# Kernel tuning notes

Measured on AMD Instinct MI355X. Metric: run time of the kernel, lower is better.

The kernel has to match this reference:

```python
import jax, jax.numpy as jnp
import numpy as np
from jax import lax

IN_CH, OC, NUM_LAYER = 6, 16, 256
ENC_DIM = OC * 4  # 64
DECODE_LEN = 23
FLAT = 5184


def _conv3d(x, w, b):
    # x: (B,C,D,H,W), w: (O,I,3,3,3), padding 1, stride 1
    y = lax.conv_general_dilated(x, w, window_strides=(1, 1, 1),
                                 padding=((1, 1), (1, 1), (1, 1)),
                                 dimension_numbers=('NCDHW', 'OIDHW', 'NCDHW'))
    return y + b[None, :, None, None, None]


def _maxpool(x):
    # MaxPool3d kernel (2,2,1) stride (2,2,1) over (D,H,W)
    return lax.reduce_window(x, -jnp.inf, lax.max,
                             (1, 1, 2, 2, 1), (1, 1, 2, 2, 1), 'VALID')


def setup_inputs() -> dict:
    key = jax.random.key(0)
    ks = jax.random.split(key, 24)
    n = lambda k, s: jax.random.normal(k, s, dtype=jnp.float32) * 0.05
    z = lambda s: jnp.zeros(s, dtype=jnp.float32)
    return {
        'x': jax.random.normal(ks[0], (512, IN_CH, 24, 72, 3), dtype=jnp.float32),
        'w1': n(ks[1], (OC, IN_CH, 3, 3, 3)), 'b1': z((OC,)),
        'w2': n(ks[2], (OC * 2, OC, 3, 3, 3)), 'b2': z((OC * 2,)),
        'w3': n(ks[3], (OC * 4, OC * 2, 3, 3, 3)), 'b3': z((OC * 4,)),
        'wih1': n(ks[4], (NUM_LAYER, ENC_DIM)), 'whh1': n(ks[5], (NUM_LAYER, NUM_LAYER)),
        'bih1': z((NUM_LAYER,)), 'bhh1': z((NUM_LAYER,)),
        'wih2': n(ks[6], (NUM_LAYER, NUM_LAYER)), 'whh2': n(ks[7], (NUM_LAYER, NUM_LAYER)),
        'bih2': z((NUM_LAYER,)), 'bhh2': z((NUM_LAYER,)),
        'w_init_h': n(ks[8], (NUM_LAYER, ENC_DIM)), 'b_init_h': z((NUM_LAYER,)),
        'w_init_h2': n(ks[9], (NUM_LAYER, NUM_LAYER)), 'b_init_h2': z((NUM_LAYER,)),
        'w_fc': n(ks[10], (1, NUM_LAYER)), 'b_fc': z((1,)),
        'w_lin1': n(ks[11], (NUM_LAYER, FLAT)), 'b_lin1': z((NUM_LAYER,)),
        'w_lin2': n(ks[12], (12, NUM_LAYER)), 'b_lin2': z((12,)),
    }


def reference(x, w1, b1, w2, b2, w3, b3,
              wih1, whh1, bih1, bhh1, wih2, whh2, bih2, bhh2,
              w_init_h, b_init_h, w_init_h2, b_init_h2,
              w_fc, b_fc, w_lin1, b_lin1, w_lin2, b_lin2):
    # Encoder: three conv+relu+pool stages (dropout is identity at p=0.0)
    out = _maxpool(jax.nn.relu(_conv3d(x, w1, b1)))
    out = _maxpool(jax.nn.relu(_conv3d(out, w2, b2)))
    out = _maxpool(jax.nn.relu(_conv3d(out, w3, b3)))  # (B, 64, 3, 9, 3)
    out = out.transpose(0, 2, 3, 4, 1)  # (B, D, H, W, C)
    B, C = out.shape[0], out.shape[-1]
    enc = out.reshape(B, -1, C)
    mean_enc = enc.mean(axis=1)  # (B, enc_dim)

    h = mean_enc @ w_init_h.T + b_init_h
    h2 = h @ w_init_h2.T + b_init_h2

    # Precompute the input-to-hidden projection once (constant across steps)
    ih_const = mean_enc @ wih1.T + bih1 + bhh1

    def step(carry, _):
        h, h2 = carry
        h_new = jnp.tanh(ih_const + h @ whh1.T)
        h2_new = jnp.tanh(h_new @ wih2.T + bih2 + h2 @ whh2.T + bhh2)
        pred = h2_new @ w_fc.T + b_fc  # (B, 1)
        return (h_new, h2_new), pred

    _, preds = lax.scan(step, (h, h2), None, length=DECODE_LEN)  # (T, B, 1)
    predictions = preds.transpose(1, 0, 2)  # (B, 23, 1)

    flat = out.reshape(B, -1)  # (B, 5184) in permuted (D,H,W,C) order, same as torch
    out_c = jnp.tanh(flat @ w_lin1.T + b_lin1) @ w_lin2.T + b_lin2  # (B, 12)
    return predictions, out_c
```

## Files before the change

### kernel.cpp

```cpp
#include <hip/hip_runtime.h>
#include <hip/hip_bf16.h>

typedef __attribute__((ext_vector_type(8))) short short8;
typedef __attribute__((ext_vector_type(4))) short short4_t;
typedef __attribute__((ext_vector_type(4))) float floatx4;

#define OFF_B1P   0
#define OFF_B2P   1792
#define OFF_B3P   8960
#define OFF_WIHT  36608
#define OFF_WIH1T 52992
#define OFF_WI2B  69376
#define OFF_WHH1B 134912
#define OFF_WIH2B 167680
#define OFF_WHH2B 200448
#define OFF_WL1P  233216
#define OFF_ME    896768
#define OFF_H0BF  929536
#define OFF_H2    1060608
#define OFF_IHC   1191680
#define OFF_P1    1322752
#define OFF_T1    1322752
#define OFF_Y     2377728
#define OFF_HSEQ  5392384
#define OFF_P2    6631168
#define OFF_P3BF  9285376

#define S2_H 88
#define S2_D 1760
#define S3_H 88
#define S3_D 1760
#define S3_HALF 14080

static __device__ inline short f2bf(float f) {
  union { __hip_bfloat16 h; short s; } u;
  u.h = __float2bfloat16(f);
  return u.s;
}
static __device__ inline float bf2f(short s) {
  union { unsigned u; float f; } v;
  v.u = ((unsigned)(unsigned short)s) << 16;
  return v.f;
}
static __device__ inline float fast_tanh(float x) {
  float e = __expf(2.f * x);
  return __builtin_fmaf(-2.f, __builtin_amdgcn_rcpf(e + 1.f), 1.f);
}

__global__ __launch_bounds__(256) void prep_kernel(
    const float* __restrict__ w1, const float* __restrict__ w2, const float* __restrict__ w3,
    const float* __restrict__ w_init_h, const float* __restrict__ wih1,
    const float* __restrict__ w_init_h2, const float* __restrict__ whh1,
    const float* __restrict__ wih2, const float* __restrict__ whh2,
    float* __restrict__ ws) {
  int i = blockIdx.x * 256 + threadIdx.x;
  if (i < 3584) {
    int j = i & 7, l = (i >> 3) & 63, c = i >> 9;
    int k = c*32 + ((l >> 4) << 3) + j;
    int tap = k >> 3, icp = k & 7, oc = l & 15;
    float v = (tap < 27 && icp < 6) ? w1[(oc*6 + icp)*27 + tap] : 0.f;
    ((__hip_bfloat16*)(ws + OFF_B1P))[i] = __float2bfloat16(v);
    return;
  }
  i -= 3584;
  if (i < 14336) {
    int j = i & 7, l = (i >> 3) & 63, cc = i >> 9;
    int c = cc % 14, nt = cc / 14;
    int k = c*32 + ((l >> 4) << 3) + j;
    int tap = k >> 4, ic = k & 15, oc = nt*16 + (l & 15);
    float v = (tap < 27) ? w2[(oc*16 + ic)*27 + tap] : 0.f;
    ((__hip_bfloat16*)(ws + OFF_B2P))[i] = __float2bfloat16(v);
    return;
  }
  i -= 14336;
  if (i < 55296) {
    int j = i & 7, l = (i >> 3) & 63, cc = i >> 9;
    int c = cc % 27, nt = cc / 27;
    int k = c*32 + ((l >> 4) << 3) + j;
    int ic = k & 31, oc = nt*16 + (l & 15);
    ((__hip_bfloat16*)(ws + OFF_B3P))[i] = __float2bfloat16(w3[(oc*32 + ic)*27 + c]);
    return;
  }
  i -= 55296;
  if (i < 16384) { int t = i & 255, k = i >> 8; ws[OFF_WIHT + i]  = w_init_h[t*64 + k];  return; }
  i -= 16384;
  if (i < 16384) { int t = i & 255, k = i >> 8; ws[OFF_WIH1T + i] = wih1[t*64 + k];      return; }
  i -= 16384;
  if (i < 65536) { ((__hip_bfloat16*)(ws + OFF_WI2B))[i] = __float2bfloat16(w_init_h2[i]); return; }
  i -= 65536;
  if (i < 65536) { ((__hip_bfloat16*)(ws + OFF_WHH1B))[i] = __float2bfloat16(whh1[i]); return; }
  i -= 65536;
  if (i < 65536) { ((__hip_bfloat16*)(ws + OFF_WIH2B))[i] = __float2bfloat16(wih2[i]); return; }
  i -= 65536;
  if (i < 65536) { ((__hip_bfloat16*)(ws + OFF_WHH2B))[i] = __float2bfloat16(whh2[i]); return; }
}

__global__ __launch_bounds__(256) void conv1_mfma(
    const float* __restrict__ x, const short* __restrict__ b1p,
    const float* __restrict__ bias, short* __restrict__ p1,
    const float* __restrict__ w_lin1, short* __restrict__ wl1p) {
  __shared__ __align__(16) short slab[8 * 38 * 5 * 8];
  int tid = threadIdx.x;
  if (blockIdx.x >= 4096) {
    int u = (blockIdx.x - 4096)*256 + tid;
    int l = u & 63, cc = u >> 6;
    int c = cc % 162, nt = cc / 162;
    int n = nt*16 + (l & 15);
    int k0 = c*32 + ((l >> 4) << 3);
    const float* src = w_lin1 + (size_t)n*5184 + k0;
    float4 v0 = *(const float4*)src;
    float4 v1 = *(const float4*)(src + 4);
    short8 s;
    s[0] = f2bf(v0.x); s[1] = f2bf(v0.y); s[2] = f2bf(v0.z); s[3] = f2bf(v0.w);
    s[4] = f2bf(v1.x); s[5] = f2bf(v1.y); s[6] = f2bf(v1.z); s[7] = f2bf(v1.w);
    *(short8*)(wl1p + (size_t)u*8) = s;
    return;
  }
  int bq = blockIdx.x >> 1, hh = blockIdx.x & 1;
  int b = bq >> 2, q = bq & 3;
  short8 z8 = {0,0,0,0,0,0,0,0};
  for (int i = tid; i < 1520; i += 256) *(short8*)(slab + i*8) = z8;
  __syncthreads();
  {
    int dslot = tid >> 5, gi = tid & 31;
    if (gi < 28) {
      int g = gi + (hh ? 26 : 0);
      int d = 6*q - 1 + dslot;
      if ((unsigned)d < 24u) {
        float4 v[6];
        #pragma unroll
        for (int ic = 0; ic < 6; ++ic)
          v[ic] = *(const float4*)(x + ((size_t)(b*6 + ic)*24 + d)*216 + g*4);
        const float* vv = (const float*)v;
        int hbase = 36*hh - 1;
        #pragma unroll
        for (int e = 0; e < 4; ++e) {
          int p = g*4 + e;
          int h = p/3, w = p - h*3;
          int r = h - hbase;
          if ((unsigned)r < 38u) {
            short8 s = z8;
            #pragma unroll
            for (int ic = 0; ic < 6; ++ic) s[ic] = f2bf(vv[ic*4 + e]);
            *(short8*)(slab + (dslot*190 + r*5 + 1 + w)*8) = s;
          }
        }
      }
    }
  }
  int lane = tid & 63, wid = tid >> 6;
  int quad = lane >> 4, col = lane & 15;
  short8 bf[7];
  #pragma unroll
  for (int c = 0; c < 7; ++c) bf[c] = *(const short8*)(b1p + (c*64 + lane)*8);
  int tapslot[7];
  #pragma unroll
  for (int c = 0; c < 7; ++c) {
    int tap = c*4 + quad;
    int tt = tap < 27 ? tap : 26;
    int kd = tt/9, rr = tt - kd*9, kh = rr/3, kw = rr - kh*3;
    tapslot[c] = kd*190 + kh*5 + kw;
  }
  float bv = bias[col];
  __syncthreads();
  for (int tile = wid; tile < 41; tile += 4) {
    int m = tile*16 + col; if (m > 647) m = 647;
    int dd = m & 1, dh = (m >> 1) & 1;
    int P = m >> 2;
    int t2 = P/3; int w = P - t2*3;
    int pdl = t2/18; int ph = t2 - pdl*18;
    int sbase = (2*pdl + dd)*190 + (2*ph + dh)*5 + w;
    floatx4 acc = {0.f, 0.f, 0.f, 0.f};
    #pragma unroll
    for (int c = 0; c < 7; ++c) {
      short8 af = *(const short8*)(slab + (sbase + tapslot[c])*8);
      acc = __builtin_amdgcn_mfma_f32_16x16x32_bf16(af, bf[c], acc, 0, 0, 0);
    }
    float v = fmaxf(fmaxf(acc[0], acc[1]), fmaxf(acc[2], acc[3]));
    v = fmaxf(v + bv, 0.f);
    int Pl = tile*4 + quad;
    if (Pl < 162) {
      int t2o = Pl/3; int wo = Pl - t2o*3;
      int pdo = t2o/18; int pho = t2o - pdo*18;
      int Pout = q*324 + hh*54 + pdo*108 + pho*3 + wo;
      p1[((size_t)b*1296 + Pout)*16 + col] = f2bf(v);
    }
  }
}

__global__ __launch_bounds__(256) void conv2_mfma(
    const short* __restrict__ p1, const short* __restrict__ b2p,
    const float* __restrict__ bias2, short* __restrict__ p2g) {
  __shared__ __align__(16) short slab[14 * S2_D];
  int tid = threadIdx.x;
  int b = blockIdx.x >> 1, qh = blockIdx.x & 1;
  short8 z8 = {0,0,0,0,0,0,0,0};
  for (int i = tid; i < 3080; i += 256) *(short8*)(slab + i*8) = z8;
  __syncthreads();
  for (int i = tid; i < 1440; i += 256) {
    int c8 = i % 6; int r = i / 6; int hr = r % 20; int d = r / 20;
    int hg = 18*qh - 1 + hr;
    if ((unsigned)hg < 36u) {
      short8 v = *(const short8*)(p1 + ((size_t)b*1296 + (d*36 + hg)*3)*16 + c8*8);
      *(short8*)(slab + (d+1)*S2_D + hr*S2_H + 16 + c8*8) = v;
    }
  }
  int lane = tid & 63, wid = tid >> 6;
  int quad = lane >> 4, col = lane & 15;
  short8 bf[2][14];
  #pragma unroll
  for (int nt = 0; nt < 2; ++nt)
    #pragma unroll
    for (int c = 0; c < 14; ++c)
      bf[nt][c] = *(const short8*)(b2p + ((nt*14 + c)*64 + lane)*8);
  int tq = quad >> 1, icoff = (quad & 1) * 8;
  int tapoff[14];
  #pragma unroll
  for (int c = 0; c < 14; ++c) {
    int tap = 2*c + tq; if (tap > 26) tap = 26;
    int kd = tap/9, rr = tap - kd*9, kh = rr/3, kw = rr - kh*3;
    tapoff[c] = kd*S2_D + kh*S2_H + kw*16 + icoff;
  }
  float bv0 = bias2[col], bv1 = bias2[16 + col];
  __syncthreads();
  for (int tile = wid; tile < 41; tile += 4) {
    int m = tile*16 + col; if (m > 647) m = 647;
    int dd = m & 1, dh = (m >> 1) & 1;
    int P = m >> 2;
    int t = P/3; int w = P - t*3;
    int pd = t/9; int phl = t - pd*9;
    int base = (2*pd + dd)*S2_D + (2*phl + dh)*S2_H + w*16;
    floatx4 a0 = {0.f,0.f,0.f,0.f}, a1 = {0.f,0.f,0.f,0.f};
    #pragma unroll
    for (int c = 0; c < 14; ++c) {
      short8 a = *(const short8*)(slab + base + tapoff[c]);
      a0 = __builtin_amdgcn_mfma_f32_16x16x32_bf16(a, bf[0][c], a0, 0, 0, 0);
      a1 = __builtin_amdgcn_mfma_f32_16x16x32_bf16(a, bf[1][c], a1, 0, 0, 0);
    }
    int P2l = tile*4 + quad;
    if (P2l < 162) {
      float v0 = fmaxf(fmaxf(fmaxf(a0[0],a0[1]), fmaxf(a0[2],a0[3])) + bv0, 0.f);
      float v1 = fmaxf(fmaxf(fmaxf(a1[0],a1[1]), fmaxf(a1[2],a1[3])) + bv1, 0.f);
      int t2 = P2l/3; int w2 = P2l - t2*3;
      int pd2 = t2/9; int ph2 = t2 - pd2*9;
      size_t off = ((size_t)b*324 + (pd2*18 + 9*qh + ph2)*3 + w2)*32;
      p2g[off + col] = f2bf(v0);
      p2g[off + 16 + col] = f2bf(v1);
    }
  }
}

__global__ __launch_bounds__(256) void conv3_mfma(
    const short* __restrict__ p2g, const short* __restrict__ b3p,
    const float* __restrict__ bias3,
    short* __restrict__ p3bf, float* __restrict__ me) {
  __shared__ __align__(16) short slab[2 * S3_HALF];
  __shared__ float smean[4][32];
  int tid = threadIdx.x;
  int b = blockIdx.x;
  short8 z8 = {0,0,0,0,0,0,0,0};
  for (int i = tid; i < 3520; i += 256) *(short8*)(slab + i*8) = z8;
  __syncthreads();
  for (int i = tid; i < 1296; i += 256) {
    int c8 = i & 1;
    int hv = (i >> 1) & 1;
    int cell = i >> 2;
    int t = cell/3; int w = cell - t*3;
    int d = t/18; int h = t - d*18;
    short8 v = *(const short8*)(p2g + ((size_t)b*324 + cell)*32 + hv*16 + c8*8);
    *(short8*)(slab + hv*S3_HALF + (d+1)*S3_D + (h+1)*S3_H + (w+1)*16 + c8*8) = v;
  }
  int lane = tid & 63, wid = tid >> 6;
  int quad = lane >> 4, col = lane & 15;
  int ntp = (wid & 1) * 2;
  int tsel = wid >> 1;
  short8 bf[2][27];
  #pragma unroll
  for (int u = 0; u < 2; ++u)
    #pragma unroll
    for (int c = 0; c < 27; ++c)
      bf[u][c] = *(const short8*)(b3p + (((ntp+u)*27 + c)*64 + lane)*8);
  const short* sb = slab + (quad >> 1)*S3_HALF + (quad & 1)*8;
  float bva = bias3[ntp*16 + col], bvb = bias3[(ntp+1)*16 + col];
  float ms0 = 0.f, ms1 = 0.f;
  __syncthreads();
  for (int tile = tsel; tile < 21; tile += 2) {
    int m = tile*16 + col; if (m > 323) m = 323;
    int dd = m & 1, dh = (m >> 1) & 1;
    int P = m >> 2;
    int t = P/3; int w = P - t*3;
    int pd = t/9; int ph = t - pd*9;
    const short* ap = sb + (2*pd + dd)*S3_D + (2*ph + dh)*S3_H + w*16;
    floatx4 a0 = {0.f,0.f,0.f,0.f}, a1 = {0.f,0.f,0.f,0.f};
    #pragma unroll
    for (int c = 0; c < 27; ++c) {
      const int kd = c/9, rr = c - kd*9, kh = rr/3, kw = rr - kh*3;
      short8 a = *(const short8*)(ap + kd*S3_D + kh*S3_H + kw*16);
      a0 = __builtin_amdgcn_mfma_f32_16x16x32_bf16(a, bf[0][c], a0, 0, 0, 0);
      a1 = __builtin_amdgcn_mfma_f32_16x16x32_bf16(a, bf[1][c], a1, 0, 0, 0);
    }
    int Pout = tile*4 + quad;
    if (Pout < 81) {
      float v0 = fmaxf(fmaxf(fmaxf(a0[0],a0[1]), fmaxf(a0[2],a0[3])) + bva, 0.f);
      float v1 = fmaxf(fmaxf(fmaxf(a1[0],a1[1]), fmaxf(a1[2],a1[3])) + bvb, 0.f);
      size_t oi = ((size_t)b*81 + Pout)*64 + ntp*16 + col;
      p3bf[oi] = f2bf(v0);
      p3bf[oi + 16] = f2bf(v1);
      ms0 += v0; ms1 += v1;
    }
  }
  ms0 += __shfl_xor(ms0, 16, 64); ms0 += __shfl_xor(ms0, 32, 64);
  ms1 += __shfl_xor(ms1, 16, 64); ms1 += __shfl_xor(ms1, 32, 64);
  if (lane < 16) { smean[wid][lane] = ms0; smean[wid][16 + lane] = ms1; }
  __syncthreads();
  if (tid < 64) {
    float s = (tid < 32) ? (smean[0][tid] + smean[2][tid])
                         : (smean[1][tid-32] + smean[3][tid-32]);
    me[b*64 + tid] = s * (1.f / 81.f);
  }
}

__global__ __launch_bounds__(256) void init_kernel(
    const float* __restrict__ me, const float* __restrict__ wiht,
    const float* __restrict__ b_init_h, const float* __restrict__ wih1t,
    const float* __restrict__ bih1, const float* __restrict__ bhh1,
    short* __restrict__ h0bf, float* __restrict__ ihcout) {
  __shared__ float sme[2][64];
  int t = threadIdx.x; int bb = blockIdx.x * 2;
  if (t < 128) sme[t >> 6][t & 63] = me[(bb + (t >> 6))*64 + (t & 63)];
  __syncthreads();
  float a0 = b_init_h[t], a1 = a0;
  float c0 = bih1[t] + bhh1[t], c1 = c0;
  #pragma unroll
  for (int k = 0; k < 64; ++k) {
    float w1v = wiht[k*256 + t], w2v = wih1t[k*256 + t];
    a0 += sme[0][k]*w1v; a1 += sme[1][k]*w1v;
    c0 += sme[0][k]*w2v; c1 += sme[1][k]*w2v;
  }
  h0bf[(size_t)bb*256 + t]     = f2bf(a0);
  h0bf[(size_t)(bb+1)*256 + t] = f2bf(a1);
  ihcout[(size_t)bb*256 + t]     = c0;
  ihcout[(size_t)(bb+1)*256 + t] = c1;
}

__global__ __launch_bounds__(512) void fusedA(
    const short* __restrict__ h0bf, const float* __restrict__ ihc,
    const short* __restrict__ whh1b, short* __restrict__ hseq,
    const short* __restrict__ p3bf, const short* __restrict__ wl1p,
    const float* __restrict__ b_lin1, float* __restrict__ t1,
    const short* __restrict__ wi2b, const float* __restrict__ b_init_h2,
    float* __restrict__ h2out) {
  __shared__ __align__(16) short pool[23040];
  int tid = threadIdx.x;

  if (blockIdx.x >= 160) {
    short (*As)[72] = (short (*)[72])pool;
    short (*Bs)[72] = (short (*)[72])(pool + 4608);
    int lane = tid & 63, w = tid >> 6;
    int quad = lane >> 4, col = lane & 15;
    int m0 = (blockIdx.x - 160) * 64;
    int n0 = w * 32;
    float bv[2];
    #pragma unroll
    for (int t = 0; t < 2; ++t) bv[t] = b_init_h2[n0 + t*16 + col];
    floatx4 acc[4][2];
    #pragma unroll
    for (int ms = 0; ms < 4; ++ms)
      #pragma unroll
      for (int t = 0; t < 2; ++t)
        #pragma unroll
        for (int r = 0; r < 4; ++r) acc[ms][t][r] = bv[t];
    int arow = tid >> 3, achk = tid & 7;
    #pragma unroll 1
    for (int kr = 0; kr < 256; kr += 64) {
      short8 ra = *(const short8*)(h0bf + (size_t)(m0 + arow)*256 + kr + achk*8);
      short8 rb[4];
      #pragma unroll
      for (int p = 0; p < 4; ++p) {
        int idx = p*512 + tid;
        rb[p] = *(const short8*)(wi2b + (size_t)(idx >> 3)*256 + kr + (idx & 7)*8);
      }
      if (kr) __syncthreads();
      *(short8*)&As[arow][achk*8] = ra;
      #pragma unroll
      for (int p = 0; p < 4; ++p) {
        int idx = p*512 + tid;
        *(short8*)&Bs[idx >> 3][(idx & 7)*8] = rb[p];
      }
      __syncthreads();
      #pragma unroll
      for (int cc = 0; cc < 2; ++cc) {
        short8 bfr[2];
        #pragma unroll
        for (int t = 0; t < 2; ++t)
          bfr[t] = *(const short8*)&Bs[n0 + t*16 + col][cc*32 + quad*8];
        #pragma unroll
        for (int ms = 0; ms < 4; ++ms) {
          short8 afr = *(const short8*)&As[ms*16 + col][cc*32 + quad*8];
          acc[ms][0] = __builtin_amdgcn_mfma_f32_16x16x32_bf16(afr, bfr[0], acc[ms][0], 0, 0, 0);
          acc[ms][1] = __builtin_amdgcn_mfma_f32_16x16x32_bf16(afr, bfr[1], acc[ms][1], 0, 0, 0);
        }
      }
    }
    #pragma unroll
    for (int ms = 0; ms < 4; ++ms)
      #pragma unroll
      for (int t = 0; t < 2; ++t)
        #pragma unroll
        for (int r = 0; r < 4; ++r)
          h2out[(size_t)(m0 + ms*16 + quad*4 + r)*256 + n0 + t*16 + col] = acc[ms][t][r];
    return;
  }

  if (blockIdx.x >= 32) {
    short (*Ab)[512][8] = (short (*)[512][8])pool;
    short (*Bb)[512][8] = (short (*)[512][8])(pool + 8192);
    int sub = tid >> 8, stid = tid & 255;
    int lane = stid & 63, w = stid >> 6;
    int quad = lane >> 4, col = lane & 15;
    int idx = (blockIdx.x - 32)*2 + sub;
    int mt = idx & 7, ntb = (idx >> 3) & 3, kz = idx >> 5;
    int c0 = (kz <= 2) ? kz*22 : 44 + (kz - 2)*20;
    int cn = (kz < 2) ? 22 : ((kz == 7) ? 18 : 20);
    int Nr = cn >> 1;
    int m0 = mt*64;
    floatx4 acc[4];
    #pragma unroll
    for (int t = 0; t < 4; ++t) {
      float bv = (kz == 0) ? b_lin1[ntb*64 + t*16 + col] : 0.f;
      #pragma unroll
      for (int r = 0; r < 4; ++r) acc[t][r] = bv;
    }
    const short* asrc = p3bf + (size_t)(m0 + w*16 + col)*5184 + c0*32 + quad*8;
    const short* bsrc = wl1p + ((size_t)((ntb*4 + w)*162 + c0)*64 + lane)*8;
    short8 ra0 = *(const short8*)asrc;
    short8 ra1 = *(const short8*)(asrc + 32);
    short8 rb0 = *(const short8*)bsrc;
    short8 rb1 = *(const short8*)(bsrc + 512);
    asrc += 64; bsrc += 1024;
    #pragma unroll 1
    for (int r = 0; r < Nr; ++r) {
      *(short8*)&Ab[0][tid][0] = ra0;
      *(short8*)&Ab[1][tid][0] = ra1;
      *(short8*)&Bb[0][tid][0] = rb0;
      *(short8*)&Bb[1][tid][0] = rb1;
      if (r + 1 < Nr) {
        ra0 = *(const short8*)asrc;
        ra1 = *(const short8*)(asrc + 32);
        rb0 = *(const short8*)bsrc;
        rb1 = *(const short8*)(bsrc + 512);
        asrc += 64; bsrc += 1024;
      }
      __syncthreads();
      #pragma unroll
      for (int cc = 0; cc < 2; ++cc) {
        short8 a = *(const short8*)&Ab[cc][sub*256 + w*64 + lane][0];
        #pragma unroll
        for (int t = 0; t < 4; ++t) {
          short8 b = *(const short8*)&Bb[cc][sub*256 + t*64 + lane][0];
          acc[t] = __builtin_amdgcn_mfma_f32_16x16x32_bf16(a, b, acc[t], 0, 0, 0);
        }
      }
      __syncthreads();
    }
    float* to = t1 + (size_t)kz * 131072;
    #pragma unroll
    for (int t = 0; t < 4; ++t)
      #pragma unroll
      for (int r = 0; r < 4; ++r)
        to[(size_t)(m0 + w*16 + quad*4 + r)*256 + ntb*64 + t*16 + col] = acc[t][r];
    return;
  }

  short (*hbuf)[16][264] = (short (*)[16][264])pool;
  int lane = tid & 63, wid = tid >> 6;
  int quad = lane >> 4, col = lane & 15;
  int bb = blockIdx.x * 16;
  int n0 = wid * 32;
  short8 w1f[2][8];
  #pragma unroll
  for (int t = 0; t < 2; ++t)
    #pragma unroll
    for (int c = 0; c < 8; ++c)
      w1f[t][c] = *(const short8*)(whh1b + (n0 + t*16 + col)*256 + c*32 + quad*8);
  floatx4 ihcr[2];
  #pragma unroll
  for (int t = 0; t < 2; ++t) {
    float4 iv = *(const float4*)(ihc + (size_t)(bb + col)*256 + n0 + t*16 + quad*4);
    ihcr[t][0] = iv.x; ihcr[t][1] = iv.y; ihcr[t][2] = iv.z; ihcr[t][3] = iv.w;
  }
  #pragma unroll
  for (int t = 0; t < 2; ++t)
    #pragma unroll
    for (int c = 0; c < 8; ++c) asm volatile("" : "+v"(w1f[t][c]));

  {
    int m = tid >> 5, c = tid & 31;
    *(short8*)&hbuf[0][m][c*8] = *(const short8*)(h0bf + (size_t)(bb + m)*256 + c*8);
  }
  __syncthreads();
  #pragma unroll 1
  for (int i = 0; i < 23; ++i) {
    int cur = i & 1;
    floatx4 a1[2];
    #pragma unroll
    for (int t = 0; t < 2; ++t) {
      a1[t][0] = ihcr[t][0]; a1[t][1] = ihcr[t][1];
      a1[t][2] = ihcr[t][2]; a1[t][3] = ihcr[t][3];
    }
    #pragma unroll
    for (int c = 0; c < 8; ++c) {
      short8 hb = *(const short8*)&hbuf[cur][col][c*32 + quad*8];
      a1[0] = __builtin_amdgcn_mfma_f32_16x16x32_bf16(w1f[0][c], hb, a1[0], 0, 0, 0);
      a1[1] = __builtin_amdgcn_mfma_f32_16x16x32_bf16(w1f[1][c], hb, a1[1], 0, 0, 0);
    }
    #pragma unroll
    for (int t = 0; t < 2; ++t) {
      short4_t pk;
      #pragma unroll
      for (int r = 0; r < 4; ++r) pk[r] = f2bf(fast_tanh(a1[t][r]));
      *(short4_t*)&hbuf[cur ^ 1][col][n0 + t*16 + quad*4] = pk;
      *(short4_t*)(hseq + ((size_t)i*512 + bb + col)*256 + n0 + t*16 + quad*4) = pk;
    }
    __syncthreads();
  }
}

__global__ __launch_bounds__(512) void fusedB(
    const short* __restrict__ hseq, const short* __restrict__ wih2b,
    const float* __restrict__ bih2, const float* __restrict__ bhh2,
    float* __restrict__ yseq,
    const float* __restrict__ t1, const float* __restrict__ w_lin2,
    const float* __restrict__ b_lin2, float* __restrict__ outc) {
  __shared__ __align__(16) short As[64][72];
  __shared__ __align__(16) short Bs[256][72];
  __shared__ float st[16][257];
  int tid = threadIdx.x;

  if (blockIdx.x < 32) {
    int bb = blockIdx.x * 16;
    for (int i = tid; i < 4096; i += 512) {
      int m = i >> 8, k = i & 255;
      size_t i0 = (size_t)(bb + m)*256 + k;
      float s = 0.f;
      #pragma unroll
      for (int z = 0; z < 8; ++z) s += t1[i0 + (size_t)z*131072];
      st[m][k] = fast_tanh(s);
    }
    __syncthreads();
    if (tid < 192) {
      int r = tid / 12, j = tid % 12;
      float s = b_lin2[j];
      #pragma unroll 1
      for (int k = 0; k < 256; ++k) s += st[r][k] * w_lin2[j*256 + k];
      outc[(size_t)(bb + r)*12 + j] = s;
    }
    return;
  }

  int lane = tid & 63, w = tid >> 6;
  int quad = lane >> 4, col = lane & 15;
  int m0 = (blockIdx.x - 32) * 64;
  int n0 = w * 32;
  float bv[2];
  #pragma unroll
  for (int t = 0; t < 2; ++t) {
    int n = n0 + t*16 + col;
    bv[t] = bih2[n] + bhh2[n];
  }
  floatx4 acc[4][2];
  #pragma unroll
  for (int ms = 0; ms < 4; ++ms)
    #pragma unroll
    for (int t = 0; t < 2; ++t)
      #pragma unroll
      for (int r = 0; r < 4; ++r) acc[ms][t][r] = bv[t];
  int arow = tid >> 3, achk = tid & 7;
  #pragma unroll 1
  for (int kr = 0; kr < 256; kr += 64) {
    short8 ra = *(const short8*)(hseq + (size_t)(m0 + arow)*256 + kr + achk*8);
    short8 rb[4];
    #pragma unroll
    for (int p = 0; p < 4; ++p) {
      int idx = p*512 + tid;
      rb[p] = *(const short8*)(wih2b + (size_t)(idx >> 3)*256 + kr + (idx & 7)*8);
    }
    if (kr) __syncthreads();
    *(short8*)&As[arow][achk*8] = ra;
    #pragma unroll
    for (int p = 0; p < 4; ++p) {
      int idx = p*512 + tid;
      *(short8*)&Bs[idx >> 3][(idx & 7)*8] = rb[p];
    }
    __syncthreads();
    #pragma unroll
    for (int cc = 0; cc < 2; ++cc) {
      short8 bfr[2];
      #pragma unroll
      for (int t = 0; t < 2; ++t)
        bfr[t] = *(const short8*)&Bs[n0 + t*16 + col][cc*32 + quad*8];
      #pragma unroll
      for (int ms = 0; ms < 4; ++ms) {
        short8 afr = *(const short8*)&As[ms*16 + col][cc*32 + quad*8];
        acc[ms][0] = __builtin_amdgcn_mfma_f32_16x16x32_bf16(afr, bfr[0], acc[ms][0], 0, 0, 0);
        acc[ms][1] = __builtin_amdgcn_mfma_f32_16x16x32_bf16(afr, bfr[1], acc[ms][1], 0, 0, 0);
      }
    }
  }
  #pragma unroll
  for (int ms = 0; ms < 4; ++ms)
    #pragma unroll
    for (int t = 0; t < 2; ++t)
      #pragma unroll
      for (int r = 0; r < 4; ++r)
        yseq[(size_t)(m0 + ms*16 + quad*4 + r)*256 + n0 + t*16 + col] = acc[ms][t][r];
}

__global__ __launch_bounds__(512) void t_h2(
    const float* __restrict__ h2in, const float* __restrict__ yseq,
    const short* __restrict__ whh2b,
    const float* __restrict__ w_fc, const float* __restrict__ b_fc,
    float* __restrict__ preds) {
  __shared__ __align__(16) short h2buf[2][16][264];
  __shared__ float predsAll[23][8][16];
  int tid = threadIdx.x;
  int lane = tid & 63, wid = tid >> 6;
  int quad = lane >> 4, col = lane & 15;
  int bb = blockIdx.x * 16;
  int n0 = wid * 32;
  short8 w3f[2][8];
  #pragma unroll
  for (int t = 0; t < 2; ++t)
    #pragma unroll
    for (int c = 0; c < 8; ++c)
      w3f[t][c] = *(const short8*)(whh2b + (n0 + t*16 + col)*256 + c*32 + quad*8);
  float4 wfcv[2];
  #pragma unroll
  for (int t = 0; t < 2; ++t)
    wfcv[t] = *(const float4*)(w_fc + n0 + t*16 + quad*4);
  float bfc = b_fc[0];
  #pragma unroll
  for (int t = 0; t < 2; ++t)
    #pragma unroll
    for (int c = 0; c < 8; ++c) asm volatile("" : "+v"(w3f[t][c]));

  for (int i = tid; i < 4096; i += 512) {
    int m = i >> 8, k = i & 255;
    h2buf[0][m][k] = f2bf(h2in[(size_t)(bb + m)*256 + k]);
  }
  __syncthreads();
  #pragma unroll 1
  for (int i = 0; i < 23; ++i) {
    int cur = i & 1;
    float4 yv[2];
    #pragma unroll
    for (int t = 0; t < 2; ++t)
      yv[t] = *(const float4*)(yseq + ((size_t)i*512 + bb + col)*256 + n0 + t*16 + quad*4);
    floatx4 z0 = {0.f,0.f,0.f,0.f}, z1 = {0.f,0.f,0.f,0.f};
    #pragma unroll
    for (int c = 0; c < 8; ++c) {
      short8 gb = *(const short8*)&h2buf[cur][col][c*32 + quad*8];
      z0 = __builtin_amdgcn_mfma_f32_16x16x32_bf16(w3f[0][c], gb, z0, 0, 0, 0);
      z1 = __builtin_amdgcn_mfma_f32_16x16x32_bf16(w3f[1][c], gb, z1, 0, 0, 0);
    }
    float pr = 0.f;
    short4_t o0, o1;
    const float* y0p = (const float*)&yv[0];
    const float* y1p = (const float*)&yv[1];
    const float* wf0 = (const float*)&wfcv[0];
    const float* wf1 = (const float*)&wfcv[1];
    #pragma unroll
    for (int r = 0; r < 4; ++r) {
      float t0 = fast_tanh(z0[r] + y0p[r]);
      float t1 = fast_tanh(z1[r] + y1p[r]);
      o0[r] = f2bf(t0); o1[r] = f2bf(t1);
      pr += t0*wf0[r] + t1*wf1[r];
    }
    *(short4_t*)&h2buf[cur ^ 1][col][n0 + quad*4] = o0;
    *(short4_t*)&h2buf[cur ^ 1][col][n0 + 16 + quad*4] = o1;
    pr += __shfl_xor(pr, 16, 64);
    pr += __shfl_xor(pr, 32, 64);
    if (lane < 16) predsAll[i][wid][lane] = pr;
    __syncthreads();
  }
  if (tid < 16) {
    #pragma unroll 1
    for (int p = 0; p < 23; ++p) {
      float sv = bfc;
      #pragma unroll
      for (int w = 0; w < 8; ++w) sv += predsAll[p][w][tid];
      preds[(size_t)(bb + tid)*23 + p] = sv;
    }
  }
}

extern "C" void kernel_launch(void* const* d_in, const int* in_sizes, int n_in,
                              void* d_out, int out_size, void* d_ws, size_t ws_size,
                              hipStream_t stream) {
  const float* x         = (const float*)d_in[0];
  const float* w1        = (const float*)d_in[1];
  const float* b1        = (const float*)d_in[2];
  const float* w2        = (const float*)d_in[3];
  const float* b2        = (const float*)d_in[4];
  const float* w3        = (const float*)d_in[5];
  const float* b3        = (const float*)d_in[6];
  const float* wih1      = (const float*)d_in[7];
  const float* whh1      = (const float*)d_in[8];
  const float* bih1      = (const float*)d_in[9];
  const float* bhh1      = (const float*)d_in[10];
  const float* wih2      = (const float*)d_in[11];
  const float* whh2      = (const float*)d_in[12];
  const float* bih2      = (const float*)d_in[13];
  const float* bhh2      = (const float*)d_in[14];
  const float* w_init_h  = (const float*)d_in[15];
  const float* b_init_h  = (const float*)d_in[16];
  const float* w_init_h2 = (const float*)d_in[17];
  const float* b_init_h2 = (const float*)d_in[18];
  const float* w_fc      = (const float*)d_in[19];
  const float* b_fc      = (const float*)d_in[20];
  const float* w_lin1    = (const float*)d_in[21];
  const float* b_lin1    = (const float*)d_in[22];
  const float* w_lin2    = (const float*)d_in[23];
  const float* b_lin2    = (const float*)d_in[24];
  float* ws  = (float*)d_ws;
  float* out = (float*)d_out;

  prep_kernel<<<1438, 256, 0, stream>>>(w1, w2, w3, w_init_h, wih1, w_init_h2,
                                        whh1, wih2, whh2, ws);
  conv1_mfma<<<4744, 256, 0, stream>>>(x, (const short*)(ws + OFF_B1P), b1,
                                       (short*)(ws + OFF_P1),
                                       w_lin1, (short*)(ws + OFF_WL1P));
  conv2_mfma<<<1024, 256, 0, stream>>>((const short*)(ws + OFF_P1),
                                       (const short*)(ws + OFF_B2P), b2,
                                       (short*)(ws + OFF_P2));
  conv3_mfma<<<512, 256, 0, stream>>>((const short*)(ws + OFF_P2),
                                      (const short*)(ws + OFF_B3P), b3,
                                      (short*)(ws + OFF_P3BF), ws + OFF_ME);
  init_kernel<<<256, 256, 0, stream>>>(ws + OFF_ME, ws + OFF_WIHT, b_init_h,
                                       ws + OFF_WIH1T, bih1, bhh1,
                                       (short*)(ws + OFF_H0BF), ws + OFF_IHC);
  fusedA<<<168, 512, 0, stream>>>((const short*)(ws + OFF_H0BF), ws + OFF_IHC,
                                  (const short*)(ws + OFF_WHH1B),
                                  (short*)(ws + OFF_HSEQ),
                                  (const short*)(ws + OFF_P3BF),
                                  (const short*)(ws + OFF_WL1P),
                                  b_lin1, ws + OFF_T1,
                                  (const short*)(ws + OFF_WI2B), b_init_h2,
                                  ws + OFF_H2);
  fusedB<<<216, 512, 0, stream>>>((const short*)(ws + OFF_HSEQ),
                                  (const short*)(ws + OFF_WIH2B),
                                  bih2, bhh2, ws + OFF_Y,
                                  ws + OFF_T1, w_lin2, b_lin2, out + 11776);
  t_h2<<<32, 512, 0, stream>>>(ws + OFF_H2, ws + OFF_Y,
                               (const short*)(ws + OFF_WHH2B),
                               w_fc, b_fc, out);
}
```

Measured before the change: 282.8 us.

## Split conv2 blocks along depth and stage w_lin2 in LDS for fusedB head

conv2 now splits each batch item into four blocks (depth half × height half) instead of two. This halves the LDS slab per block and doubles the grid, which should raise occupancy and parallelism, at the cost of reloading halo rows in depth. In fusedB, the shared arrays are merged into one byte pool aliased differently per branch, shrinking LDS footprint. The small lin2 head now caches w_lin2 in padded LDS and unrolls its dot-product loop, instead of reading it from global memory each iteration.

```diff
diff --git a/kernel.cpp b/kernel.cpp
--- a/kernel.cpp
+++ b/kernel.cpp
@@ -191,18 +191,19 @@
 __global__ __launch_bounds__(256) void conv2_mfma(
     const short* __restrict__ p1, const short* __restrict__ b2p,
     const float* __restrict__ bias2, short* __restrict__ p2g) {
-  __shared__ __align__(16) short slab[14 * S2_D];
+  __shared__ __align__(16) short slab[8 * S2_D];
   int tid = threadIdx.x;
-  int b = blockIdx.x >> 1, qh = blockIdx.x & 1;
+  int b = blockIdx.x >> 2, qd = (blockIdx.x >> 1) & 1, qh = blockIdx.x & 1;
   short8 z8 = {0,0,0,0,0,0,0,0};
-  for (int i = tid; i < 3080; i += 256) *(short8*)(slab + i*8) = z8;
-  __syncthreads();
-  for (int i = tid; i < 1440; i += 256) {
-    int c8 = i % 6; int r = i / 6; int hr = r % 20; int d = r / 20;
+  for (int i = tid; i < 1760; i += 256) *(short8*)(slab + i*8) = z8;
+  __syncthreads();
+  for (int i = tid; i < 960; i += 256) {
+    int c8 = i % 6; int r = i / 6; int hr = r % 20; int dslot = r / 20;
     int hg = 18*qh - 1 + hr;
-    if ((unsigned)hg < 36u) {
-      short8 v = *(const short8*)(p1 + ((size_t)b*1296 + (d*36 + hg)*3)*16 + c8*8);
-      *(short8*)(slab + (d+1)*S2_D + hr*S2_H + 16 + c8*8) = v;
+    int dg = 6*qd - 1 + dslot;
+    if ((unsigned)hg < 36u && (unsigned)dg < 12u) {
+      short8 v = *(const short8*)(p1 + ((size_t)b*1296 + (dg*36 + hg)*3)*16 + c8*8);
+      *(short8*)(slab + dslot*S2_D + hr*S2_H + 16 + c8*8) = v;
     }
   }
   int lane = tid & 63, wid = tid >> 6;
@@ -223,13 +224,13 @@
   }
   float bv0 = bias2[col], bv1 = bias2[16 + col];
   __syncthreads();
-  for (int tile = wid; tile < 41; tile += 4) {
-    int m = tile*16 + col; if (m > 647) m = 647;
+  for (int tile = wid; tile < 21; tile += 4) {
+    int m = tile*16 + col; if (m > 323) m = 323;
     int dd = m & 1, dh = (m >> 1) & 1;
     int P = m >> 2;
     int t = P/3; int w = P - t*3;
-    int pd = t/9; int phl = t - pd*9;
-    int base = (2*pd + dd)*S2_D + (2*phl + dh)*S2_H + w*16;
+    int pdl = t/9; int phl = t - pdl*9;
+    int base = (2*pdl + dd)*S2_D + (2*phl + dh)*S2_H + w*16;
     floatx4 a0 = {0.f,0.f,0.f,0.f}, a1 = {0.f,0.f,0.f,0.f};
     #pragma unroll
     for (int c = 0; c < 14; ++c) {
@@ -238,11 +239,12 @@
       a1 = __builtin_amdgcn_mfma_f32_16x16x32_bf16(a, bf[1][c], a1, 0, 0, 0);
     }
     int P2l = tile*4 + quad;
-    if (P2l < 162) {
+    if (P2l < 81) {
       float v0 = fmaxf(fmaxf(fmaxf(a0[0],a0[1]), fmaxf(a0[2],a0[3])) + bv0, 0.f);
       float v1 = fmaxf(fmaxf(fmaxf(a1[0],a1[1]), fmaxf(a1[2],a1[3])) + bv1, 0.f);
       int t2 = P2l/3; int w2 = P2l - t2*3;
-      int pd2 = t2/9; int ph2 = t2 - pd2*9;
+      int pdl2 = t2/9; int ph2 = t2 - pdl2*9;
+      int pd2 = pdl2 + 3*qd;
       size_t off = ((size_t)b*324 + (pd2*18 + 9*qh + ph2)*3 + w2)*32;
       p2g[off + col] = f2bf(v0);
       p2g[off + 16 + col] = f2bf(v1);
@@ -532,13 +534,17 @@
     float* __restrict__ yseq,
     const float* __restrict__ t1, const float* __restrict__ w_lin2,
     const float* __restrict__ b_lin2, float* __restrict__ outc) {
-  __shared__ __align__(16) short As[64][72];
-  __shared__ __align__(16) short Bs[256][72];
-  __shared__ float st[16][257];
+  __shared__ __align__(16) unsigned char poolB[46080];
   int tid = threadIdx.x;
 
   if (blockIdx.x < 32) {
+    float (*st)[257] = (float (*)[257])poolB;
+    float* swl = (float*)(poolB + 16448);
     int bb = blockIdx.x * 16;
+    for (int i = tid; i < 3072; i += 512) {
+      int j = i >> 8, k = i & 255;
+      swl[j*260 + k] = w_lin2[i];
+    }
     for (int i = tid; i < 4096; i += 512) {
       int m = i >> 8, k = i & 255;
       size_t i0 = (size_t)(bb + m)*256 + k;
@@ -551,13 +557,15 @@
     if (tid < 192) {
       int r = tid / 12, j = tid % 12;
       float s = b_lin2[j];
-      #pragma unroll 1
-      for (int k = 0; k < 256; ++k) s += st[r][k] * w_lin2[j*256 + k];
+      #pragma unroll 8
+      for (int k = 0; k < 256; ++k) s += st[r][k] * swl[j*260 + k];
       outc[(size_t)(bb + r)*12 + j] = s;
     }
     return;
   }
 
+  short (*As)[72] = (short (*)[72])poolB;
+  short (*Bs)[72] = (short (*)[72])(poolB + 9216);
   int lane = tid & 63, w = tid >> 6;
   int quad = lane >> 4, col = lane & 15;
   int m0 = (blockIdx.x - 32) * 64;
@@ -730,7 +738,7 @@
   conv1_mfma<<<4744, 256, 0, stream>>>(x, (const short*)(ws + OFF_B1P), b1,
                                        (short*)(ws + OFF_P1),
                                        w_lin1, (short*)(ws + OFF_WL1P));
-  conv2_mfma<<<1024, 256, 0, stream>>>((const short*)(ws + OFF_P1),
+  conv2_mfma<<<2048, 256, 0, stream>>>((const short*)(ws + OFF_P1),
                                        (const short*)(ws + OFF_B2P), b2,
                                        (short*)(ws + OFF_P2));
   conv3_mfma<<<512, 256, 0, stream>>>((const short*)(ws + OFF_P2),
```

Result: faster. 269.2 us (-4.8%).
